# Kernel tuning notes

Hardware: AMD Instinct MI355X
Metric: run time of the kernel (lower is better)

The kernel has to match this reference:

```python
import jax, jax.numpy as jnp
import numpy as np
from jax import lax

NEG = -1e9


def cyk(scores, lens):
    """Inside algorithm (logsumexp semiring) for a span tree-CRF.
    scores: [B, N, N]; scores[b, i, j] = potential of right-closed span [i, j].
    lens:   [B] int sentence lengths.
    Returns logZ[b] = inside score of span [0, lens[b]-1].
    Chart A[b, i, w] = inside score of span starting at i with width w.
    Recurrence: A[i, w] = D[i, w] + logsumexp_{u=1..w-1}(A[i, u] + A[i+u, w-u]).
    """
    B, N = scores.shape[0], scores.shape[1]
    i = jnp.arange(N)
    u = jnp.arange(N + 1)
    # D[b, i, w] = scores[b, i, i+w-1] (span of width w starting at i)
    j_end = jnp.clip(i[:, None] + u[None, :] - 1, 0, N - 1)          # [N, N+1]
    D = jnp.take_along_axis(scores, j_end[None], axis=2)             # [B, N, N+1]
    valid_span = (u[None, :] >= 1) & (i[:, None] + u[None, :] <= N)  # [N, N+1]
    D = jnp.where(valid_span[None], D, NEG)

    A = jnp.full((B, N, N + 1), NEG, scores.dtype)
    A = A.at[:, :, 1].set(D[:, :, 1])  # width-1 spans
    rowc = jnp.clip(i[:, None] + u[None, :], 0, N - 1)               # [N, N+1]

    def step(A, w):
        colc = jnp.broadcast_to(jnp.clip(w - u, 0, N), (N, N + 1))
        right = A[:, rowc, colc]                                     # A[b, i+u, w-u]
        ok = (u[None, :] >= 1) & (u[None, :] <= w - 1) & (i[:, None] + u[None, :] <= N - 1)
        tmp = jnp.where(ok[None], A + right, NEG)                    # splits over u
        new = jax.nn.logsumexp(tmp, axis=-1) + D[:, :, w]
        return A.at[:, :, w].set(new), None

    A, _ = lax.scan(step, A, jnp.arange(2, N + 1))
    return jnp.take_along_axis(A[:, 0, :], lens[:, None], axis=1)[:, 0]


def setup_inputs() -> dict:
    key = jax.random.key(0)
    k1, k2 = jax.random.split(key)
    B, N = 64, 256
    span_logits = jax.random.normal(k1, (B, N, N, 2), jnp.float32)
    spans_ind = jax.random.randint(k2, (B, N, N), 0, 3).astype(jnp.int32)
    maskspan = jnp.ones((B, N, N), bool)
    span_mask = jnp.zeros((B, N, N), bool)
    return {"span_logits": span_logits, "spans_ind": spans_ind,
            "maskspan": maskspan, "span_mask": span_mask}


def reference(span_logits, spans_ind, maskspan, span_mask):
    # spans_ind: values>0 shifted down by 1, then to bool (gold span indicator)
    sind = jnp.where(spans_ind > 0, spans_ind - 1, spans_ind).astype(bool)
    # hard masking path (smoothing == 1.0, norm == False, ent_lamb == 0.0)
    s0 = jnp.where(span_mask | sind, NEG, span_logits[..., 0])
    s1 = jnp.where(span_mask | ~sind, NEG, span_logits[..., 1])
    ob = jnp.logaddexp(s0, s1)                                  # gold-constrained potentials
    allv = jnp.logaddexp(span_logits[..., 0], span_logits[..., 1])  # unconstrained
    lens = maskspan[:, 0].sum(-1).astype(jnp.int32)
    marginals = cyk(ob, lens)
    logz = cyk(allv, lens)
    return (logz - marginals).sum() / maskspan[:, 0].sum().astype(span_logits.dtype)
```

## Files before the change

kernel.cpp:

```cpp
#include <hip/hip_runtime.h>


#define NN 256
#define BATCH 64
#define NCHART (2 * BATCH)
#define NEGV -1000000000.0f
#define NEGB -1.0e30f
#define K2f 1.4426950408889634f
#define LN2f 0.6931471805599453f

#define CHARTF 32896
#define CMAXF 260
#define BB_OFF (CHARTF + CMAXF)
#define FLG_OFF (BB_OFF + 16)
#define SCR_OFF (FLG_OFF + 260)
#define SCRF 3952
#define LDSF (SCR_OFF + SCRF)

#define RES_OFF ((size_t)16)
#define LEN_OFF ((size_t)(16 + NCHART))
#define FB_OFF  ((size_t)(16 + NCHART + BATCH + 16))

__device__ __forceinline__ float fexp2(float x) {
#if __has_builtin(__builtin_amdgcn_exp2f)
    return __builtin_amdgcn_exp2f(x);
#else
    return exp2f(x);
#endif
}

__device__ __forceinline__ float wave_max64(float x) {
    int v = __float_as_int(x);
    int s;
    s = __builtin_amdgcn_update_dpp(v, v, 0x111, 0xf, 0xf, false);
    v = __float_as_int(fmaxf(__int_as_float(v), __int_as_float(s)));
    s = __builtin_amdgcn_update_dpp(v, v, 0x112, 0xf, 0xf, false);
    v = __float_as_int(fmaxf(__int_as_float(v), __int_as_float(s)));
    s = __builtin_amdgcn_update_dpp(v, v, 0x114, 0xf, 0xf, false);
    v = __float_as_int(fmaxf(__int_as_float(v), __int_as_float(s)));
    s = __builtin_amdgcn_update_dpp(v, v, 0x118, 0xf, 0xf, false);
    v = __float_as_int(fmaxf(__int_as_float(v), __int_as_float(s)));
    s = __builtin_amdgcn_update_dpp(v, v, 0x142, 0xa, 0xf, false);
    v = __float_as_int(fmaxf(__int_as_float(v), __int_as_float(s)));
    s = __builtin_amdgcn_update_dpp(v, v, 0x143, 0xc, 0xf, false);
    v = __float_as_int(fmaxf(__int_as_float(v), __int_as_float(s)));
    return __int_as_float(__builtin_amdgcn_readlane(v, 63));
}

__device__ __forceinline__ float rlane(float v, int idx) {
    return __int_as_float(__builtin_amdgcn_readlane(__float_as_int(v), idx));
}

__device__ __forceinline__ int cstart(int v) {
    return 257 * (v - 1) - ((v * (v - 1)) >> 1);
}

__device__ __forceinline__ float score_at(const float* __restrict__ logits,
                                          const int* __restrict__ spans_ind,
                                          const void* __restrict__ span_mask,
                                          int isb, int t, int b, int i, int j) {
    size_t sidx = ((size_t)b * NN + i) * NN + j;
    float l0 = logits[2 * sidx];
    float l1 = logits[2 * sidx + 1];
    if (t) {
        float mx = fmaxf(l0, l1), mn = fminf(l0, l1);
        return mx + log1pf(__expf(mn - mx));
    } else {
        bool sind = (spans_ind[sidx] == 2);
        bool sm = isb ? (((const unsigned char*)span_mask)[sidx] != 0)
                      : (((const int*)span_mask)[sidx] != 0);
        float s0 = (sm || sind)  ? NEGV : l0;
        float s1 = (sm || !sind) ? NEGV : l1;
        float mx = fmaxf(s0, s1), mn = fminf(s0, s1);
        return mx + log1pf(__expf(mn - mx));
    }
}

template <int KK>
__device__ __forceinline__ void group8(
    float* __restrict__ Lc, float* __restrict__ scr, float* __restrict__ cm,
    float* __restrict__ bbuf, int* flg, float* __restrict__ sres,
    int W, int tid, int wave, int lane, int lenv) {
    const int ES = 257 - W;

    {
        const int p  = wave >> 2;
        const int sp = wave & 3;
        const int g0 = 2 * p, g1 = g0 + 1;
        const int L0 = W + g0, L1 = W + g1;
        const bool has1 = (L1 <= 256);
        const int E0 = 257 - L0;
        const int E1 = has1 ? (257 - L1) : 0;

        float b0 = NEGB, b1 = NEGB;
        for (int uu = g0 + 1 + lane; uu <= W - 1; uu += 64)
            b0 = fmaxf(b0, cm[uu] + cm[L0 - uu]);
        b0 = wave_max64(b0);
        if (has1) {
            for (int uu = g1 + 1 + lane; uu <= W - 1; uu += 64)
                b1 = fmaxf(b1, cm[uu] + cm[L1 - uu]);
            b1 = wave_max64(b1);
        }
        if (lane == 0 && sp == 0) {
            bbuf[g0] = b0;
            if (has1) bbuf[g1] = b1;
        }

        const int n = W - 1 - g0;
        const int C = (n + 3) >> 2;
        const int ua = g0 + 1 + sp * C;
        const int ub = min(ua + C - 1, W - 1);
        const int R = ub - ua + 1;

        float su0r, su1r;
        {
            int u = ua + lane;
            int uc = (u <= ub) ? u : ub;
            bool v0 = (lane < R);
            bool v1 = v0 && has1 && (uc >= g1 + 1);
            float e0 = fexp2(cm[uc] + cm[L0 - uc] - b0);
            float e1 = fexp2(cm[uc] + cm[L1 - uc] - b1);
            su0r = v0 ? e0 : 0.f;
            su1r = v1 ? e1 : 0.f;
        }

        float acc0[KK], acc1[KK];
#pragma unroll
        for (int k = 0; k < KK; ++k) { acc0[k] = 0.f; acc1[k] = 0.f; }

        if (R > 0) {
            int la  = cstart(ua) + lane;
            int ra0 = cstart(L0 - ua) + ua + lane;
            int ra1 = cstart(L1 - ua) + ua + lane;
            int A  = 257 - ua;
            int B0 = 257 - (L0 - ua);
            int B1 = 257 - (L1 - ua);
#pragma unroll 2
            for (int idx = 0; idx < R; ++idx) {
                float su0 = rlane(su0r, idx);
                float su1 = rlane(su1r, idx);
#pragma unroll
                for (int k = 0; k < KK; ++k) {
                    float lv = Lc[la  + 64 * k];
                    float r0 = Lc[ra0 + 64 * k];
                    float r1 = Lc[ra1 + 64 * k];
                    acc0[k] = fmaf(su0 * lv, r0, acc0[k]);
                    acc1[k] = fmaf(su1 * lv, r1, acc1[k]);
                }
                la += A; A -= 1;
                ra0 -= B0; B0 += 1;
                ra1 -= B1; B1 += 1;
            }
        }

        const int s0 = 4 * p + (sp & 1);
        const int s1 = s0 + 2;
        if (sp >= 2) {
#pragma unroll
            for (int k = 0; k < KK; ++k) {
                int ge = lane + 64 * k;
                if (ge < E0) scr[s0 * ES + ge] = acc0[k];
                if (ge < E1) scr[s1 * ES + ge] = acc1[k];
            }
        }
        __syncthreads();
        if (sp < 2) {
#pragma unroll
            for (int k = 0; k < KK; ++k) {
                int ge = lane + 64 * k;
                if (ge < E0) scr[s0 * ES + ge] += acc0[k];
                if (ge < E1) scr[s1 * ES + ge] += acc1[k];
            }
        }
    }
    __syncthreads();

    if (wave < 8) {
        const int g = wave;
        const int L = W + g;
        if (L <= 256) {
            const int E = 257 - L;
            float m = bbuf[g];

            float s[KK];
#pragma unroll
            for (int k = 0; k < KK; ++k) {
                int ge = lane + 64 * k;
                s[k] = (ge < E) ? scr[(2 * g) * ES + ge] +
                                  scr[(2 * g + 1) * ES + ge]
                                : 0.f;
            }

            for (int j = g; j >= 1; --j) {
                const int v = L - j;
                while (((volatile int*)flg)[v] == 0) {}
                asm volatile("" ::: "memory");
                float pm = cm[j] + cm[v];
                float nm = fmaxf(m, pm);
                float sc = fexp2(m - nm), pj = fexp2(pm - nm);
                const int cj = cstart(j), cl = cstart(v);
#pragma unroll
                for (int k = 0; k < KK; ++k) {
                    int ge = lane + 64 * k;
                    if (ge < E) {
                        float tt = Lc[cj + ge] * Lc[cl + ge + j] +
                                   Lc[cl + ge] * Lc[cj + ge + v];
                        s[k] = fmaf(s[k], sc, pj * tt);
                    }
                }
                m = nm;
            }

            float xa[KK];
            float mx = NEGB;
#pragma unroll
            for (int k = 0; k < KK; ++k) {
                int ge = lane + 64 * k;
                float av = NEGB;
                if (ge < E) av = Lc[cstart(L) + ge] + m + __log2f(s[k]);
                xa[k] = av;
                mx = fmaxf(mx, av);
            }
            mx = wave_max64(mx);
#pragma unroll
            for (int k = 0; k < KK; ++k) {
                int ge = lane + 64 * k;
                if (ge < E) Lc[cstart(L) + ge] = fexp2(xa[k] - mx);
            }
            if (lane == 0) {
                cm[L] = mx;
                if (L == lenv) *sres = xa[0];
            }
            __threadfence_block();
            asm volatile("" ::: "memory");
            if (lane == 0) ((volatile int*)flg)[L] = 1;
        }
    }
    __syncthreads();
}

__device__ __forceinline__ void level_direct(
    float* __restrict__ Lc, float* __restrict__ cm,
    float* __restrict__ swm, float* __restrict__ sres,
    int w, int tid, int wave, int lane, int lenv) {
    const int E = NN + 1 - w;
    float a = NEGB;
    if (tid < E) {
        float b0 = NEGB;
        for (int u = 1; u <= w - 1; ++u) b0 = fmaxf(b0, cm[u] + cm[w - u]);
        float s = 0.f;
        for (int u = 1; u <= w - 1; ++u) {
            float su = fexp2(cm[u] + cm[w - u] - b0);
            s = fmaf(su * Lc[cstart(u) + tid], Lc[cstart(w - u) + u + tid], s);
        }
        int ad = cstart(w) + tid;
        a = Lc[ad] + b0 + __log2f(s);
        Lc[ad] = a;
        if (tid == 0 && w == lenv) *sres = a;
    }
    float m = wave_max64(a);
    if (lane == 0) swm[wave] = m;
    __syncthreads();
    float cmw = swm[0];
#pragma unroll
    for (int i = 1; i < 16; ++i) cmw = fmaxf(cmw, swm[i]);
    if (tid < E) {
        int ad = cstart(w) + tid;
        Lc[ad] = fexp2(Lc[ad] - cmw);
    }
    if (tid == 0) cm[w] = cmw;
    __syncthreads();
}

template <bool USE_LDS>
__global__ __launch_bounds__(1024) void cyk_kernel(
    const float* __restrict__ logits,
    const int* __restrict__ spans_ind,
    const void* __restrict__ maskspan,
    const void* __restrict__ span_mask,
    float* __restrict__ ws) {
    extern __shared__ float lds[];
    const int c = blockIdx.x;
    const int b = c >> 1;
    const int t = c & 1;
    const int tid = threadIdx.x;
    const int wave = tid >> 6, lane = tid & 63;

    float* __restrict__ Lc = USE_LDS ? lds : (ws + FB_OFF + (size_t)c * LDSF);
    float* __restrict__ cm = Lc + CHARTF;
    float* __restrict__ bbuf = Lc + BB_OFF;
    int* flg = (int*)(Lc + FLG_OFF);
    float* __restrict__ scr = Lc + SCR_OFF;

    __shared__ int s_len;
    __shared__ int s_isb;
    __shared__ float s_wmax[16];
    __shared__ float s_res;
    if (tid == 0) {
        s_len = 0;
        s_res = K2f * NEGV;
        unsigned probe = *(const unsigned*)maskspan;
        s_isb = (probe > 1u) ? 1 : 0;
    }
    if (tid < 260) flg[tid] = 0;
    __syncthreads();
    const int isb = s_isb;

    if (tid < NN) {
        size_t off = (size_t)b * NN * NN + tid;
        int v = isb ? (((const unsigned char*)maskspan)[off] ? 1 : 0)
                    : (((const int*)maskspan)[off] ? 1 : 0);
        atomicAdd(&s_len, v);
    }

    for (int it = 0; it < 64; ++it) {
        int f = (it << 10) + tid;
        int i = f >> 8, j = f & 255;
        if (j >= i) {
            float sc = score_at(logits, spans_ind, span_mask, isb, t, b, i, j);
            Lc[cstart(j - i + 1) + i] = K2f * sc;
        }
    }
    __syncthreads();
    const int lenv = s_len;

    {
        float a = (tid < NN) ? Lc[tid] : NEGB;
        if (tid == 0 && lenv == 1) s_res = a;
        float m = wave_max64(a);
        if (lane == 0) s_wmax[wave] = m;
        __syncthreads();
        float c1 = s_wmax[0];
#pragma unroll
        for (int i = 1; i < 16; ++i) c1 = fmaxf(c1, s_wmax[i]);
        if (tid < NN) Lc[tid] = fexp2(a - c1);
        if (tid == 0) cm[1] = c1;
    }
    __syncthreads();

    for (int w = 2; w <= 9; ++w)
        level_direct(Lc, cm, s_wmax, &s_res, w, tid, wave, lane, lenv);
    for (int W = 10; W <= 58; W += 8)
        group8<4>(Lc, scr, cm, bbuf, flg, &s_res, W, tid, wave, lane, lenv);
    for (int W = 66; W <= 122; W += 8)
        group8<3>(Lc, scr, cm, bbuf, flg, &s_res, W, tid, wave, lane, lenv);
    for (int W = 130; W <= 186; W += 8)
        group8<2>(Lc, scr, cm, bbuf, flg, &s_res, W, tid, wave, lane, lenv);
    for (int W = 194; W <= 250; W += 8)
        group8<1>(Lc, scr, cm, bbuf, flg, &s_res, W, tid, wave, lane, lenv);

    if (tid == 0) {
        int len = s_len;
        float rres = (len >= 1) ? (s_res * LN2f) : NEGV;
        ws[RES_OFF + c] = rres;
        if (t == 0) ws[LEN_OFF + b] = (float)len;
    }
}

__global__ __launch_bounds__(64) void finish_kernel(const float* __restrict__ ws,
                                                    float* __restrict__ out) {
    int b = threadIdx.x;
    float diff = ws[RES_OFF + 2 * b + 1] - ws[RES_OFF + 2 * b];
    float len  = ws[LEN_OFF + b];
    for (int d = 32; d > 0; d >>= 1) {
        diff += __shfl_xor(diff, d);
        len  += __shfl_xor(len, d);
    }
    if (b == 0) out[0] = diff / len;
}

extern "C" void kernel_launch(void* const* d_in, const int* in_sizes, int n_in,
                              void* d_out, int out_size, void* d_ws, size_t ws_size,
                              hipStream_t stream) {
    const float* logits    = (const float*)d_in[0];
    const int*   spans_ind = (const int*)d_in[1];
    const void*  maskspan  = d_in[2];
    const void*  span_mask = d_in[3];
    float* ws = (float*)d_ws;

    const size_t shbytes = (size_t)LDSF * sizeof(float);
    hipError_t e = hipFuncSetAttribute(
        reinterpret_cast<const void*>(&cyk_kernel<true>),
        hipFuncAttributeMaxDynamicSharedMemorySize, (int)shbytes);
    if (e == hipSuccess) {
        hipLaunchKernelGGL(cyk_kernel<true>, dim3(NCHART), dim3(1024), shbytes,
                           stream, logits, spans_ind, maskspan, span_mask, ws);
    } else {
        hipLaunchKernelGGL(cyk_kernel<false>, dim3(NCHART), dim3(1024), 0,
                           stream, logits, spans_ind, maskspan, span_mask, ws);
    }
    hipLaunchKernelGGL(finish_kernel, dim3(1), dim3(64), 0, stream,
                       ws, (float*)d_out);
}
```

Measured before the change: 476.5 us.

## Overlap next group's bulk split sums with current group's dependent tail

```diff
diff --git a/kernel.cpp b/kernel.cpp
--- a/kernel.cpp
+++ b/kernel.cpp
@@ -9,13 +9,13 @@
 #define K2f 1.4426950408889634f
 #define LN2f 0.6931471805599453f
 
-#define CHARTF 32896
-#define CMAXF 260
-#define BB_OFF (CHARTF + CMAXF)
+#define CM_OFF  32896
+#define BB_OFF  (CM_OFF + 257)
 #define FLG_OFF (BB_OFF + 16)
-#define SCR_OFF (FLG_OFF + 260)
-#define SCRF 3952
-#define LDSF (SCR_OFF + SCRF)
+#define MSC_OFF (FLG_OFF + 257)
+#define S0_OFF  (MSC_OFF + 3)
+#define S1_OFF  (S0_OFF + 3696)
+#define LDSF    (S1_OFF + 3824)
 
 #define RES_OFF ((size_t)16)
 #define LEN_OFF ((size_t)(16 + NCHART))
@@ -76,119 +76,170 @@
     }
 }
 
-template <int KK>
-__device__ __forceinline__ void group8(
-    float* __restrict__ Lc, float* __restrict__ scr, float* __restrict__ cm,
-    float* __restrict__ bbuf, int* flg, float* __restrict__ sres,
-    int W, int tid, int wave, int lane, int lenv) {
-    const int ES = 257 - W;
-
-    {
-        const int p  = wave >> 2;
-        const int sp = wave & 3;
-        const int g0 = 2 * p, g1 = g0 + 1;
-        const int L0 = W + g0, L1 = W + g1;
-        const bool has1 = (L1 <= 256);
-        const int E0 = 257 - L0;
-        const int E1 = has1 ? (257 - L1) : 0;
-
-        float b0 = NEGB, b1 = NEGB;
-        for (int uu = g0 + 1 + lane; uu <= W - 1; uu += 64)
-            b0 = fmaxf(b0, cm[uu] + cm[L0 - uu]);
-        b0 = wave_max64(b0);
-        if (has1) {
-            for (int uu = g1 + 1 + lane; uu <= W - 1; uu += 64)
-                b1 = fmaxf(b1, cm[uu] + cm[L1 - uu]);
+template <int KK, int KK2>
+__device__ __forceinline__ void group_olap(
+    float* __restrict__ Lc, float* __restrict__ cm, int* flg, int* msc,
+    const float* __restrict__ scrR, float* __restrict__ scrW,
+    const float* __restrict__ bbR, float* __restrict__ bbW,
+    int W, int wave, int lane, int lenv) {
+    const int ESR = 257 - W;
+
+    if (wave >= 8) {
+        if constexpr (KK2 > 0) {
+            const int W2 = W + 8;
+            const int ESW = 257 - W2;
+            const int p = (wave - 8) >> 1, sp = (wave - 8) & 1;
+            const int G0 = 2 * p, G1 = G0 + 1;
+            const int L0 = W2 + G0, L1 = W2 + G1;
+            const bool has1 = (L1 <= 256);
+            const int E0 = 257 - L0;
+            const int E1 = has1 ? (257 - L1) : 0;
+            const int lo0 = G0 + 9, hi = W2 - 9;
+
+            float b0 = NEGB, b1 = NEGB;
+            for (int uu = lo0 + lane; uu <= hi; uu += 64) {
+                float cu = cm[uu];
+                b0 = fmaxf(b0, cu + cm[L0 - uu]);
+                if (uu >= lo0 + 1) b1 = fmaxf(b1, cu + cm[L1 - uu]);
+            }
+            b0 = wave_max64(b0);
             b1 = wave_max64(b1);
+            if (lane == 0 && sp == 0) { bbW[G0] = b0; bbW[G1] = b1; }
+
+            const int n = hi - lo0 + 1;
+            if (n > 0) {
+                const int C = (n + 1) >> 1;
+                const int ua = lo0 + sp * C;
+                const int ub = min(ua + C - 1, hi);
+                const int R = ub - ua + 1;
+
+                float su0r, su1r;
+                {
+                    int u = ua + lane;
+                    int uc = (u <= ub) ? u : ub;
+                    bool v0 = (lane < R);
+                    bool v1 = v0 && has1 && (uc >= lo0 + 1);
+                    float e0 = fexp2(cm[uc] + cm[L0 - uc] - b0);
+                    float e1 = fexp2(cm[uc] + cm[L1 - uc] - b1);
+                    su0r = v0 ? e0 : 0.f;
+                    su1r = v1 ? e1 : 0.f;
+                }
+                float su2r = 0.f, su3r = 0.f;
+                if (R > 64) {
+                    int u = ua + 64 + lane;
+                    int uc = (u <= ub) ? u : ub;
+                    bool v0 = (64 + lane < R);
+                    bool v1 = v0 && has1;
+                    float e0 = fexp2(cm[uc] + cm[L0 - uc] - b0);
+                    float e1 = fexp2(cm[uc] + cm[L1 - uc] - b1);
+                    su2r = v0 ? e0 : 0.f;
+                    su3r = v1 ? e1 : 0.f;
+                }
+
+                float a0[KK2], a1[KK2];
+#pragma unroll
+                for (int k = 0; k < KK2; ++k) { a0[k] = 0.f; a1[k] = 0.f; }
+
+                if (R > 0) {
+                    int la  = cstart(ua) + lane;
+                    int ra0 = cstart(L0 - ua) + ua + lane;
+                    int ra1 = cstart(L1 - ua) + ua + lane;
+                    int A  = 257 - ua;
+                    int B0 = 257 - (L0 - ua);
+                    int B1 = 257 - (L1 - ua);
+                    const int R0 = (R < 64) ? R : 64;
+#pragma unroll 2
+                    for (int idx = 0; idx < R0; ++idx) {
+                        float su0 = rlane(su0r, idx);
+                        float su1 = rlane(su1r, idx);
+#pragma unroll
+                        for (int k = 0; k < KK2; ++k) {
+                            float lv = Lc[la  + 64 * k];
+                            float r0 = Lc[ra0 + 64 * k];
+                            float r1 = Lc[ra1 + 64 * k];
+                            a0[k] = fmaf(su0 * lv, r0, a0[k]);
+                            a1[k] = fmaf(su1 * lv, r1, a1[k]);
+                        }
+                        la += A; A -= 1;
+                        ra0 -= B0; B0 += 1;
+                        ra1 -= B1; B1 += 1;
+                    }
+#pragma unroll 2
+                    for (int idx = 64; idx < R; ++idx) {
+                        float su0 = rlane(su2r, idx - 64);
+                        float su1 = rlane(su3r, idx - 64);
+#pragma unroll
+                        for (int k = 0; k < KK2; ++k) {
+                            float lv = Lc[la  + 64 * k];
+                            float r0 = Lc[ra0 + 64 * k];
+                            float r1 = Lc[ra1 + 64 * k];
+                            a0[k] = fmaf(su0 * lv, r0, a0[k]);
+                            a1[k] = fmaf(su1 * lv, r1, a1[k]);
+                        }
+                        la += A; A -= 1;
+                        ra0 -= B0; B0 += 1;
+                        ra1 -= B1; B1 += 1;
+                    }
+                }
+#pragma unroll
+                for (int k = 0; k < KK2; ++k) {
+                    int ge = lane + 64 * k;
+                    if (ge < E0) scrW[(2 * G0 + sp) * ESW + ge] = a0[k];
+                    if (ge < E1) scrW[(2 * G1 + sp) * ESW + ge] = a1[k];
+                }
+            }
         }
-        if (lane == 0 && sp == 0) {
-            bbuf[g0] = b0;
-            if (has1) bbuf[g1] = b1;
-        }
-
-        const int n = W - 1 - g0;
-        const int C = (n + 3) >> 2;
-        const int ua = g0 + 1 + sp * C;
-        const int ub = min(ua + C - 1, W - 1);
-        const int R = ub - ua + 1;
-
-        float su0r, su1r;
-        {
-            int u = ua + lane;
-            int uc = (u <= ub) ? u : ub;
-            bool v0 = (lane < R);
-            bool v1 = v0 && has1 && (uc >= g1 + 1);
-            float e0 = fexp2(cm[uc] + cm[L0 - uc] - b0);
-            float e1 = fexp2(cm[uc] + cm[L1 - uc] - b1);
-            su0r = v0 ? e0 : 0.f;
-            su1r = v1 ? e1 : 0.f;
-        }
-
-        float acc0[KK], acc1[KK];
-#pragma unroll
-        for (int k = 0; k < KK; ++k) { acc0[k] = 0.f; acc1[k] = 0.f; }
-
-        if (R > 0) {
-            int la  = cstart(ua) + lane;
-            int ra0 = cstart(L0 - ua) + ua + lane;
-            int ra1 = cstart(L1 - ua) + ua + lane;
-            int A  = 257 - ua;
-            int B0 = 257 - (L0 - ua);
-            int B1 = 257 - (L1 - ua);
-#pragma unroll 2
-            for (int idx = 0; idx < R; ++idx) {
-                float su0 = rlane(su0r, idx);
-                float su1 = rlane(su1r, idx);
-#pragma unroll
-                for (int k = 0; k < KK; ++k) {
-                    float lv = Lc[la  + 64 * k];
-                    float r0 = Lc[ra0 + 64 * k];
-                    float r1 = Lc[ra1 + 64 * k];
-                    acc0[k] = fmaf(su0 * lv, r0, acc0[k]);
-                    acc1[k] = fmaf(su1 * lv, r1, acc1[k]);
-                }
-                la += A; A -= 1;
-                ra0 -= B0; B0 += 1;
-                ra1 -= B1; B1 += 1;
-            }
-        }
-
-        const int s0 = 4 * p + (sp & 1);
-        const int s1 = s0 + 2;
-        if (sp >= 2) {
-#pragma unroll
-            for (int k = 0; k < KK; ++k) {
-                int ge = lane + 64 * k;
-                if (ge < E0) scr[s0 * ES + ge] = acc0[k];
-                if (ge < E1) scr[s1 * ES + ge] = acc1[k];
-            }
-        }
-        __syncthreads();
-        if (sp < 2) {
-#pragma unroll
-            for (int k = 0; k < KK; ++k) {
-                int ge = lane + 64 * k;
-                if (ge < E0) scr[s0 * ES + ge] += acc0[k];
-                if (ge < E1) scr[s1 * ES + ge] += acc1[k];
-            }
-        }
-    }
-    __syncthreads();
-
-    if (wave < 8) {
+    } else {
         const int g = wave;
         const int L = W + g;
         if (L <= 256) {
             const int E = 257 - L;
-            float m = bbuf[g];
-
+            float m = NEGB;
             float s[KK];
 #pragma unroll
-            for (int k = 0; k < KK; ++k) {
-                int ge = lane + 64 * k;
-                s[k] = (ge < E) ? scr[(2 * g) * ES + ge] +
-                                  scr[(2 * g + 1) * ES + ge]
-                                : 0.f;
+            for (int k = 0; k < KK; ++k) s[k] = 0.f;
+
+            if (W >= g + 18) {
+                m = bbR[g];
+#pragma unroll
+                for (int k = 0; k < KK; ++k) {
+                    int ge = lane + 64 * k;
+                    if (ge < E)
+                        s[k] = scrR[(2 * g) * ESR + ge] +
+                               scrR[(2 * g + 1) * ESR + ge];
+                }
+            }
+
+            const int b1lo = g + 1, b1hi = min(g + 8, W - 1);
+            const int b2lo = max(W - 8, g + 9), b2hi = W - 1;
+            float m2 = m;
+            for (int u = b1lo; u <= b1hi; ++u) m2 = fmaxf(m2, cm[u] + cm[L - u]);
+            for (int u = b2lo; u <= b2hi; ++u) m2 = fmaxf(m2, cm[u] + cm[L - u]);
+            {
+                float sc = fexp2(m - m2);
+#pragma unroll
+                for (int k = 0; k < KK; ++k) s[k] *= sc;
+                m = m2;
+            }
+            for (int u = b1lo; u <= b1hi; ++u) {
+                float su = fexp2(cm[u] + cm[L - u] - m);
+                const int ca = cstart(u), cb = cstart(L - u);
+#pragma unroll
+                for (int k = 0; k < KK; ++k) {
+                    int ge = lane + 64 * k;
+                    if (ge < E)
+                        s[k] = fmaf(su * Lc[ca + ge], Lc[cb + ge + u], s[k]);
+                }
+            }
+            for (int u = b2lo; u <= b2hi; ++u) {
+                float su = fexp2(cm[u] + cm[L - u] - m);
+                const int ca = cstart(u), cb = cstart(L - u);
+#pragma unroll
+                for (int k = 0; k < KK; ++k) {
+                    int ge = lane + 64 * k;
+                    if (ge < E)
+                        s[k] = fmaf(su * Lc[ca + ge], Lc[cb + ge + u], s[k]);
+                }
             }
 
             for (int j = g; j >= 1; --j) {
@@ -229,7 +280,7 @@
             }
             if (lane == 0) {
                 cm[L] = mx;
-                if (L == lenv) *sres = xa[0];
+                if (L == lenv) ((float*)msc)[2] = xa[0];
             }
             __threadfence_block();
             asm volatile("" ::: "memory");
@@ -241,7 +292,7 @@
 
 __device__ __forceinline__ void level_direct(
     float* __restrict__ Lc, float* __restrict__ cm,
-    float* __restrict__ swm, float* __restrict__ sres,
+    float* __restrict__ swm, int* msc,
     int w, int tid, int wave, int lane, int lenv) {
     const int E = NN + 1 - w;
     float a = NEGB;
@@ -256,7 +307,7 @@
         int ad = cstart(w) + tid;
         a = Lc[ad] + b0 + __log2f(s);
         Lc[ad] = a;
-        if (tid == 0 && w == lenv) *sres = a;
+        if (tid == 0 && w == lenv) ((float*)msc)[2] = a;
     }
     float m = wave_max64(a);
     if (lane == 0) swm[wave] = m;
@@ -287,30 +338,33 @@
     const int wave = tid >> 6, lane = tid & 63;
 
     float* __restrict__ Lc = USE_LDS ? lds : (ws + FB_OFF + (size_t)c * LDSF);
-    float* __restrict__ cm = Lc + CHARTF;
-    float* __restrict__ bbuf = Lc + BB_OFF;
+    float* __restrict__ cm = Lc + CM_OFF;
+    float* __restrict__ BB = Lc + BB_OFF;
     int* flg = (int*)(Lc + FLG_OFF);
-    float* __restrict__ scr = Lc + SCR_OFF;
-
-    __shared__ int s_len;
-    __shared__ int s_isb;
-    __shared__ float s_wmax[16];
-    __shared__ float s_res;
+    int* msc = (int*)(Lc + MSC_OFF);
+    float* __restrict__ S0 = Lc + S0_OFF;
+    float* __restrict__ S1 = Lc + S1_OFF;
+
     if (tid == 0) {
-        s_len = 0;
-        s_res = K2f * NEGV;
+        ((float*)msc)[2] = K2f * NEGV;
         unsigned probe = *(const unsigned*)maskspan;
-        s_isb = (probe > 1u) ? 1 : 0;
-    }
-    if (tid < 260) flg[tid] = 0;
-    __syncthreads();
-    const int isb = s_isb;
-
-    if (tid < NN) {
-        size_t off = (size_t)b * NN * NN + tid;
-        int v = isb ? (((const unsigned char*)maskspan)[off] ? 1 : 0)
-                    : (((const int*)maskspan)[off] ? 1 : 0);
-        atomicAdd(&s_len, v);
+        msc[1] = (probe > 1u) ? 1 : 0;
+    }
+    if (tid < 257) flg[tid] = 0;
+    __syncthreads();
+    const int isb = msc[1];
+
+    if (wave == 0) {
+        int cnt = 0;
+        for (int q = 0; q < 4; ++q) {
+            int j = lane * 4 + q;
+            size_t off = (size_t)b * NN * NN + j;
+            int v = isb ? (((const unsigned char*)maskspan)[off] ? 1 : 0)
+                        : (((const int*)maskspan)[off] ? 1 : 0);
+            cnt += v;
+        }
+        for (int d = 32; d; d >>= 1) cnt += __shfl_xor(cnt, d);
+        if (lane == 0) msc[0] = cnt;
     }
 
     for (int it = 0; it < 64; ++it) {
@@ -322,36 +376,48 @@
         }
     }
     __syncthreads();
-    const int lenv = s_len;
+    const int lenv = msc[0];
 
     {
         float a = (tid < NN) ? Lc[tid] : NEGB;
-        if (tid == 0 && lenv == 1) s_res = a;
+        if (tid == 0 && lenv == 1) ((float*)msc)[2] = a;
         float m = wave_max64(a);
-        if (lane == 0) s_wmax[wave] = m;
+        if (lane == 0) BB[wave] = m;
         __syncthreads();
-        float c1 = s_wmax[0];
-#pragma unroll
-        for (int i = 1; i < 16; ++i) c1 = fmaxf(c1, s_wmax[i]);
+        float c1 = BB[0];
+#pragma unroll
+        for (int i = 1; i < 16; ++i) c1 = fmaxf(c1, BB[i]);
         if (tid < NN) Lc[tid] = fexp2(a - c1);
         if (tid == 0) cm[1] = c1;
     }
     __syncthreads();
 
     for (int w = 2; w <= 9; ++w)
-        level_direct(Lc, cm, s_wmax, &s_res, w, tid, wave, lane, lenv);
-    for (int W = 10; W <= 58; W += 8)
-        group8<4>(Lc, scr, cm, bbuf, flg, &s_res, W, tid, wave, lane, lenv);
-    for (int W = 66; W <= 122; W += 8)
-        group8<3>(Lc, scr, cm, bbuf, flg, &s_res, W, tid, wave, lane, lenv);
-    for (int W = 130; W <= 186; W += 8)
-        group8<2>(Lc, scr, cm, bbuf, flg, &s_res, W, tid, wave, lane, lenv);
-    for (int W = 194; W <= 250; W += 8)
-        group8<1>(Lc, scr, cm, bbuf, flg, &s_res, W, tid, wave, lane, lenv);
+        level_direct(Lc, cm, BB, msc, w, tid, wave, lane, lenv);
+
+#define GRP(KA, KB, WV)                                                     \
+    {                                                                       \
+        const int gk = ((WV) - 10) >> 3;                                    \
+        const float* sR = (gk & 1) ? S1 : S0;                               \
+        float* sW = (gk & 1) ? S0 : S1;                                     \
+        const float* bR = BB + (gk & 1) * 8;                                \
+        float* bW = BB + ((gk + 1) & 1) * 8;                                \
+        group_olap<KA, KB>(Lc, cm, flg, msc, sR, sW, bR, bW, (WV),          \
+                           wave, lane, lenv);                               \
+    }
+    for (int W = 10; W <= 50; W += 8) GRP(4, 4, W)
+    GRP(4, 3, 58)
+    for (int W = 66; W <= 114; W += 8) GRP(3, 3, W)
+    GRP(3, 2, 122)
+    for (int W = 130; W <= 178; W += 8) GRP(2, 2, W)
+    GRP(2, 1, 186)
+    for (int W = 194; W <= 242; W += 8) GRP(1, 1, W)
+    GRP(1, 0, 250)
+#undef GRP
 
     if (tid == 0) {
-        int len = s_len;
-        float rres = (len >= 1) ? (s_res * LN2f) : NEGV;
+        int len = msc[0];
+        float rres = (len >= 1) ? (((float*)msc)[2] * LN2f) : NEGV;
         ws[RES_OFF + c] = rres;
         if (t == 0) ws[LEN_OFF + b] = (float)len;
     }
```

Measured after the change: 420.9 us. 1.13x faster.
